# Kernel optimization log

Hardware: AMD Instinct MI355X
Metric: run time of the kernel (lower is better)

The kernel has to match this reference:

```python
import jax, jax.numpy as jnp
import numpy as np

X_DIM, Y_DIM, HIDDEN, N = 768, 768, 300, 768


def setup_inputs() -> dict:
    key = jax.random.key(0)
    ks = jax.random.split(key, 7)
    lim1 = 1.0 / np.sqrt(X_DIM + Y_DIM)
    lim2 = 1.0 / np.sqrt(HIDDEN)
    return {
        "x_samples": jax.random.normal(ks[0], (N, X_DIM), dtype=jnp.float32),
        "y_samples": jax.random.normal(ks[1], (N, Y_DIM), dtype=jnp.float32),
        "perm": jax.random.permutation(ks[2], N).astype(jnp.int32),
        # Linear 1: (x_dim+y_dim) -> hidden, torch default uniform init
        "W1": jax.random.uniform(ks[3], (HIDDEN, X_DIM + Y_DIM), jnp.float32, -lim1, lim1),
        "b1": jax.random.uniform(ks[4], (HIDDEN,), jnp.float32, -lim1, lim1),
        # Linear 2: hidden -> 1
        "W2": jax.random.uniform(ks[5], (1, HIDDEN), jnp.float32, -lim2, lim2),
        "b2": jax.random.uniform(ks[6], (1,), jnp.float32, -lim2, lim2),
    }


def reference(x_samples, y_samples, perm, W1, b1, W2, b2):
    n = x_samples.shape[0]
    x_dim = x_samples.shape[1]
    # First linear is separable across the concat: split W1 into x- and y-parts.
    hx = x_samples @ W1[:, :x_dim].T            # [N, H]
    hy = y_samples @ W1[:, x_dim:].T            # [N, H]
    w2 = W2[0]                                   # [H]
    # T0: matched pairs (x_i, y_i)
    t0 = jax.nn.softplus(jax.nn.relu(hx + hy + b1) @ w2 + b2[0])   # [N]
    # T1[i, j] = F(x_j, y_perm[i]) -- pairwise tile, [N, N, H] intermediate
    hyp = hy[perm]                               # [N, H]
    hpair = jax.nn.relu(hyp[:, None, :] + hx[None, :, :] + b1)     # [N, N, H]
    t1 = jax.nn.softplus(hpair @ w2 + b2[0])     # [N, N]
    lower_bound = t0.mean() - (jax.nn.logsumexp(t1, axis=1).mean() - jnp.log(n).astype(t1.dtype))
    return lower_bound
```

## Files before the change

kernel.cpp:

```cpp
#include <hip/hip_runtime.h>
#include <math.h>

#define NN   768
#define HH   300
#define KD   768

#define P_OFF    0
#define PKS_STR  245760
#define PG_STR   1966080
#define CF_OFF   3932160
#define AF_OFF   4177920
#define RS_OFF   4423680
#define T0_OFF   4435968

__global__ __launch_bounds__(256) void k1_gemm(
    const float* __restrict__ x, const float* __restrict__ y,
    const int* __restrict__ perm, const float* __restrict__ W1,
    float* __restrict__ wsf)
{
    const int tid = threadIdx.x;
    const int tx = tid & 15;
    const int ty = tid >> 4;
    const int i0 = blockIdx.x * 128;
    const int h0 = blockIdx.y * 64;
    const int g  = blockIdx.z & 1;
    const int ks = blockIdx.z >> 1;
    const int kbeg = ks * 96;

    const float* src = g ? y : x;
    const int koff = g ? KD : 0;

    __shared__ float Xt[32][132];
    __shared__ float Wt[32][68];

    float4 acc[4][2];
    #pragma unroll
    for (int r = 0; r < 4; ++r) { acc[r][0] = make_float4(0,0,0,0);
                                  acc[r][1] = make_float4(0,0,0,0); }

    const int kq = (tid & 7) << 2;
    const float* xp[4];
    int xr[4];
    #pragma unroll
    for (int it = 0; it < 4; ++it) {
        int row = ((tid + it*256) >> 3);
        int gr = i0 + row;
        if (g) gr = perm[gr];
        xp[it] = src + (size_t)gr * KD + kbeg + kq;
        xr[it] = row;
    }
    const float* wp[2];
    int wr[2]; bool wv[2];
    #pragma unroll
    for (int it = 0; it < 2; ++it) {
        int hrow = ((tid + it*256) >> 3);
        int hg = h0 + hrow;
        wv[it] = hg < HH;
        wp[it] = W1 + (size_t)(wv[it] ? hg : 0) * (2*KD) + koff + kbeg + kq;
        wr[it] = hrow;
    }

    for (int kb = 0; kb < 96; kb += 32) {
        float4 xv[4], wvv[2];
        #pragma unroll
        for (int it = 0; it < 4; ++it) xv[it] = *(const float4*)(xp[it] + kb);
        #pragma unroll
        for (int it = 0; it < 2; ++it) {
            wvv[it] = *(const float4*)(wp[it] + kb);
            if (!wv[it]) wvv[it] = make_float4(0,0,0,0);
        }
        if (kb) __syncthreads();
        #pragma unroll
        for (int it = 0; it < 4; ++it) {
            Xt[kq+0][xr[it]] = xv[it].x; Xt[kq+1][xr[it]] = xv[it].y;
            Xt[kq+2][xr[it]] = xv[it].z; Xt[kq+3][xr[it]] = xv[it].w;
        }
        #pragma unroll
        for (int it = 0; it < 2; ++it) {
            Wt[kq+0][wr[it]] = wvv[it].x; Wt[kq+1][wr[it]] = wvv[it].y;
            Wt[kq+2][wr[it]] = wvv[it].z; Wt[kq+3][wr[it]] = wvv[it].w;
        }
        __syncthreads();

        #pragma unroll 8
        for (int k = 0; k < 32; ++k) {
            float4 a  = *(const float4*)&Wt[k][4*ty];
            float4 b0 = *(const float4*)&Xt[k][4*tx];
            float4 b1v = *(const float4*)&Xt[k][64 + 4*tx];
            float ar[4] = {a.x, a.y, a.z, a.w};
            #pragma unroll
            for (int r = 0; r < 4; ++r) {
                acc[r][0].x = fmaf(ar[r], b0.x,  acc[r][0].x);
                acc[r][0].y = fmaf(ar[r], b0.y,  acc[r][0].y);
                acc[r][0].z = fmaf(ar[r], b0.z,  acc[r][0].z);
                acc[r][0].w = fmaf(ar[r], b0.w,  acc[r][0].w);
                acc[r][1].x = fmaf(ar[r], b1v.x, acc[r][1].x);
                acc[r][1].y = fmaf(ar[r], b1v.y, acc[r][1].y);
                acc[r][1].z = fmaf(ar[r], b1v.z, acc[r][1].z);
                acc[r][1].w = fmaf(ar[r], b1v.w, acc[r][1].w);
            }
        }
    }

    float* dst = wsf + P_OFF + (size_t)(g*8 + ks) * PKS_STR;
    #pragma unroll
    for (int r = 0; r < 4; ++r) {
        float* rp = dst + (size_t)(h0 + 4*ty + r) * NN + i0;
        *(float4*)(rp + 4*tx)      = acc[r][0];
        *(float4*)(rp + 64 + 4*tx) = acc[r][1];
    }
}

__global__ __launch_bounds__(256) void k1b_combine(
    const float* __restrict__ b1, float* __restrict__ wsf)
{
    int idx = blockIdx.x * 256 + threadIdx.x;
    int g = idx >= 61440;
    int rem = idx - g * 61440;
    int h = rem / 192;
    int i4 = (rem % 192) * 4;

    float4 o = make_float4(0.f,0.f,0.f,0.f);
    if (h < HH) {
        const float* p = wsf + P_OFF + (size_t)g * PG_STR + (size_t)h * NN + i4;
        #pragma unroll
        for (int ks = 0; ks < 8; ++ks) {
            float4 v = *(const float4*)(p + (size_t)ks * PKS_STR);
            o.x += v.x; o.y += v.y; o.z += v.z; o.w += v.w;
        }
        if (g) {
            float bv = b1[h];
            o.x += bv; o.y += bv; o.z += bv; o.w += bv;
        }
    }
    float* dst = wsf + (g ? AF_OFF : CF_OFF) + (size_t)h * NN + i4;
    *(float4*)dst = o;
}

__global__ __launch_bounds__(256) void k2_pair(
    const float* __restrict__ wsf, const float* __restrict__ w2,
    const int* __restrict__ perm, const float* __restrict__ b2,
    float* __restrict__ rsO, float* __restrict__ t0c)
{
    const int tid = threadIdx.x;
    const int tx = tid & 15;
    const int ty = tid >> 4;
    const int j0 = blockIdx.x * 48;
    const int i0 = blockIdx.y * 48;

    const float* AF = wsf + AF_OFF;
    const float* CF = wsf + CF_OFF;

    __shared__ float As[50][48];
    __shared__ float Cs[50][48];
    __shared__ float w2s[50];

    int ho[3], qo[3]; bool val[3];
    #pragma unroll
    for (int s = 0; s < 3; ++s) {
        int e = tid + s * 256;
        val[s] = e < 600;
        ho[s] = e / 12;
        qo[s] = (e % 12) * 4;
    }

    float acc[3][3];
    #pragma unroll
    for (int r = 0; r < 3; ++r)
        #pragma unroll
        for (int c = 0; c < 3; ++c) acc[r][c] = 0.f;

    float4 pa[3] = {}, pc[3] = {};
    #pragma unroll
    for (int s = 0; s < 3; ++s) if (val[s]) {
        pa[s] = *(const float4*)(AF + (size_t)ho[s] * NN + i0 + qo[s]);
        pc[s] = *(const float4*)(CF + (size_t)ho[s] * NN + j0 + qo[s]);
    }
    float pw = (tid < 50) ? w2[tid] : 0.f;

    for (int cc = 0; cc < 6; ++cc) {
        if (cc) __syncthreads();
        #pragma unroll
        for (int s = 0; s < 3; ++s) if (val[s]) {
            *(float4*)&As[ho[s]][qo[s]] = pa[s];
            *(float4*)&Cs[ho[s]][qo[s]] = pc[s];
        }
        if (tid < 50) w2s[tid] = pw;
        __syncthreads();

        if (cc < 5) {
            const float* a = AF + (size_t)(cc + 1) * 50 * NN;
            const float* c = CF + (size_t)(cc + 1) * 50 * NN;
            #pragma unroll
            for (int s = 0; s < 3; ++s) if (val[s]) {
                pa[s] = *(const float4*)(a + (size_t)ho[s] * NN + i0 + qo[s]);
                pc[s] = *(const float4*)(c + (size_t)ho[s] * NN + j0 + qo[s]);
            }
            if (tid < 50) pw = w2[(cc + 1) * 50 + tid];
        }

        #pragma unroll 5
        for (int h = 0; h < 50; ++h) {
            float wh = w2s[h];
            float ar[3] = {As[h][ty], As[h][ty + 16], As[h][ty + 32]};
            float cr[3] = {Cs[h][tx], Cs[h][tx + 16], Cs[h][tx + 32]};
            #pragma unroll
            for (int r = 0; r < 3; ++r)
                #pragma unroll
                for (int c = 0; c < 3; ++c)
                    acc[r][c] = fmaf(fmaxf(ar[r] + cr[c], 0.f), wh, acc[r][c]);
        }
    }

    const float b2v = b2[0];
    #pragma unroll
    for (int r = 0; r < 3; ++r) {
        int i = i0 + ty + 16 * r;
        int pj = perm[i];
        float rsum = 0.f;
        #pragma unroll
        for (int c = 0; c < 3; ++c) {
            int j = j0 + tx + 16 * c;
            float u = acc[r][c] + b2v;
            rsum += expf(u);
            if (j == pj)
                t0c[i] = (u > 0.f) ? u + log1pf(expf(-u)) : log1pf(expf(u));
        }
        #pragma unroll
        for (int off = 8; off; off >>= 1)
            rsum += __shfl_xor(rsum, off, 16);
        if (tx == 0) rsO[(size_t)blockIdx.x * NN + i] = rsum;
    }
}

__global__ __launch_bounds__(256) void k3_final(
    const float* __restrict__ wsf, float* __restrict__ out)
{
    const int tid = threadIdx.x;
    const float* rs = wsf + RS_OFF;
    const float* t0 = wsf + T0_OFF;

    double st0 = 0.0, slse = 0.0;
    for (int i = tid; i < NN; i += 256) {
        float s = 0.f;
        #pragma unroll
        for (int jb = 0; jb < 16; ++jb) s += rs[(size_t)jb * NN + i];
        st0  += (double)t0[i];
        slse += log((double)NN + (double)s);
    }
    __shared__ double sa[256], sb[256];
    sa[tid] = st0; sb[tid] = slse;
    __syncthreads();
    for (int s = 128; s > 0; s >>= 1) {
        if (tid < s) { sa[tid] += sa[tid+s]; sb[tid] += sb[tid+s]; }
        __syncthreads();
    }
    if (tid == 0) {
        double lb = sa[0]/(double)NN - (sb[0]/(double)NN - log((double)NN));
        out[0] = (float)lb;
    }
}

extern "C" void kernel_launch(void* const* d_in, const int* in_sizes, int n_in,
                              void* d_out, int out_size, void* d_ws, size_t ws_size,
                              hipStream_t stream) {
    const float* x    = (const float*)d_in[0];
    const float* y    = (const float*)d_in[1];
    const int*   perm = (const int*)  d_in[2];
    const float* W1   = (const float*)d_in[3];
    const float* b1   = (const float*)d_in[4];
    const float* W2   = (const float*)d_in[5];
    const float* b2   = (const float*)d_in[6];
    float* wsf = (float*)d_ws;
    float* out = (float*)d_out;

    k1_gemm    <<<dim3(6,5,16), 256, 0, stream>>>(x, y, perm, W1, wsf);
    k1b_combine<<<480,          256, 0, stream>>>(b1, wsf);
    k2_pair    <<<dim3(16,16),  256, 0, stream>>>(wsf, W2, perm, b2,
                                                  wsf + RS_OFF, wsf + T0_OFF);
    k3_final   <<<1,            256, 0, stream>>>(wsf, out);
}
```

Measured before the change: 129.1 us.

## Store hidden activations row-major with padded hidden dim for vectorized pair kernel

Changes the intermediate hx/hy buffers from hidden-major [H][N] to sample-major [N][320] with hidden padded to 320. The GEMM epilogue writes transposed float4s, the combine kernel reduces along the new layout, and the pair kernel loads whole hidden chunks of 152 per sample into shared memory and reads float4 along hidden. The aim is fewer shared-memory load instructions and fewer sync phases in the pair kernel (2 chunks instead of 6). The trade-off is larger shared memory per block (~60KB), which may lower occupancy, and possible bank conflicts with the 156-float row stride.

```diff
diff --git a/kernel.cpp b/kernel.cpp
--- a/kernel.cpp
+++ b/kernel.cpp
@@ -3,6 +3,7 @@
 
 #define NN   768
 #define HH   300
+#define HP   320
 #define KD   768
 
 #define P_OFF    0
@@ -33,10 +34,11 @@
     __shared__ float Xt[32][132];
     __shared__ float Wt[32][68];
 
-    float4 acc[4][2];
-    #pragma unroll
-    for (int r = 0; r < 4; ++r) { acc[r][0] = make_float4(0,0,0,0);
-                                  acc[r][1] = make_float4(0,0,0,0); }
+    float acc[4][8];
+    #pragma unroll
+    for (int r = 0; r < 4; ++r)
+        #pragma unroll
+        for (int cc = 0; cc < 8; ++cc) acc[r][cc] = 0.f;
 
     const int kq = (tid & 7) << 2;
     const float* xp[4];
@@ -88,26 +90,21 @@
             float4 b0 = *(const float4*)&Xt[k][4*tx];
             float4 b1v = *(const float4*)&Xt[k][64 + 4*tx];
             float ar[4] = {a.x, a.y, a.z, a.w};
+            float br[8] = {b0.x, b0.y, b0.z, b0.w, b1v.x, b1v.y, b1v.z, b1v.w};
             #pragma unroll
-            for (int r = 0; r < 4; ++r) {
-                acc[r][0].x = fmaf(ar[r], b0.x,  acc[r][0].x);
-                acc[r][0].y = fmaf(ar[r], b0.y,  acc[r][0].y);
-                acc[r][0].z = fmaf(ar[r], b0.z,  acc[r][0].z);
-                acc[r][0].w = fmaf(ar[r], b0.w,  acc[r][0].w);
-                acc[r][1].x = fmaf(ar[r], b1v.x, acc[r][1].x);
-                acc[r][1].y = fmaf(ar[r], b1v.y, acc[r][1].y);
-                acc[r][1].z = fmaf(ar[r], b1v.z, acc[r][1].z);
-                acc[r][1].w = fmaf(ar[r], b1v.w, acc[r][1].w);
-            }
+            for (int r = 0; r < 4; ++r)
+                #pragma unroll
+                for (int cc = 0; cc < 8; ++cc)
+                    acc[r][cc] = fmaf(ar[r], br[cc], acc[r][cc]);
         }
     }
 
     float* dst = wsf + P_OFF + (size_t)(g*8 + ks) * PKS_STR;
     #pragma unroll
-    for (int r = 0; r < 4; ++r) {
-        float* rp = dst + (size_t)(h0 + 4*ty + r) * NN + i0;
-        *(float4*)(rp + 4*tx)      = acc[r][0];
-        *(float4*)(rp + 64 + 4*tx) = acc[r][1];
+    for (int cc = 0; cc < 8; ++cc) {
+        int i = i0 + ((cc >> 2) ? 64 : 0) + 4*tx + (cc & 3);
+        float4 v = make_float4(acc[0][cc], acc[1][cc], acc[2][cc], acc[3][cc]);
+        *(float4*)(dst + (size_t)i * HP + h0 + 4*ty) = v;
     }
 }
 
@@ -117,23 +114,21 @@
     int idx = blockIdx.x * 256 + threadIdx.x;
     int g = idx >= 61440;
     int rem = idx - g * 61440;
-    int h = rem / 192;
-    int i4 = (rem % 192) * 4;
+    int i = rem / 80;
+    int h4 = (rem % 80) * 4;
 
     float4 o = make_float4(0.f,0.f,0.f,0.f);
-    if (h < HH) {
-        const float* p = wsf + P_OFF + (size_t)g * PG_STR + (size_t)h * NN + i4;
-        #pragma unroll
-        for (int ks = 0; ks < 8; ++ks) {
-            float4 v = *(const float4*)(p + (size_t)ks * PKS_STR);
-            o.x += v.x; o.y += v.y; o.z += v.z; o.w += v.w;
-        }
-        if (g) {
-            float bv = b1[h];
-            o.x += bv; o.y += bv; o.z += bv; o.w += bv;
-        }
-    }
-    float* dst = wsf + (g ? AF_OFF : CF_OFF) + (size_t)h * NN + i4;
+    const float* p = wsf + P_OFF + (size_t)g * PG_STR + (size_t)i * HP + h4;
+    #pragma unroll
+    for (int ks = 0; ks < 8; ++ks) {
+        float4 v = *(const float4*)(p + (size_t)ks * PKS_STR);
+        o.x += v.x; o.y += v.y; o.z += v.z; o.w += v.w;
+    }
+    if (g && h4 < HH) {
+        float4 bv = *(const float4*)(b1 + h4);
+        o.x += bv.x; o.y += bv.y; o.z += bv.z; o.w += bv.w;
+    }
+    float* dst = wsf + (g ? AF_OFF : CF_OFF) + (size_t)i * HP + h4;
     *(float4*)dst = o;
 }
 
@@ -151,17 +146,14 @@
     const float* AF = wsf + AF_OFF;
     const float* CF = wsf + CF_OFF;
 
-    __shared__ float As[50][48];
-    __shared__ float Cs[50][48];
-    __shared__ float w2s[50];
-
-    int ho[3], qo[3]; bool val[3];
-    #pragma unroll
-    for (int s = 0; s < 3; ++s) {
-        int e = tid + s * 256;
-        val[s] = e < 600;
-        ho[s] = e / 12;
-        qo[s] = (e % 12) * 4;
+    __shared__ __align__(16) float As[48][156];
+    __shared__ __align__(16) float Cs[48][156];
+    __shared__ __align__(16) float w2s[304];
+
+    if (tid < 76) {
+        float4 wv = make_float4(0.f,0.f,0.f,0.f);
+        if (tid < 75) wv = *(const float4*)(w2 + 4*tid);
+        *(float4*)&w2s[4*tid] = wv;
     }
 
     float acc[3][3];
@@ -170,45 +162,51 @@
         #pragma unroll
         for (int c = 0; c < 3; ++c) acc[r][c] = 0.f;
 
-    float4 pa[3] = {}, pc[3] = {};
-    #pragma unroll
-    for (int s = 0; s < 3; ++s) if (val[s]) {
-        pa[s] = *(const float4*)(AF + (size_t)ho[s] * NN + i0 + qo[s]);
-        pc[s] = *(const float4*)(CF + (size_t)ho[s] * NN + j0 + qo[s]);
-    }
-    float pw = (tid < 50) ? w2[tid] : 0.f;
-
-    for (int cc = 0; cc < 6; ++cc) {
-        if (cc) __syncthreads();
-        #pragma unroll
-        for (int s = 0; s < 3; ++s) if (val[s]) {
-            *(float4*)&As[ho[s]][qo[s]] = pa[s];
-            *(float4*)&Cs[ho[s]][qo[s]] = pc[s];
-        }
-        if (tid < 50) w2s[tid] = pw;
+    #pragma unroll
+    for (int ch = 0; ch < 2; ++ch) {
+        const int hbeg = ch * 152;
+        const int nq = ch ? 37 : 38;
+        if (ch) __syncthreads();
+        for (int e = tid; e < 48 * nq; e += 256) {
+            int i = e / nq, q = e % nq;
+            *(float4*)&As[i][4*q] =
+                *(const float4*)(AF + (size_t)(i0 + i) * HP + hbeg + 4*q);
+            *(float4*)&Cs[i][4*q] =
+                *(const float4*)(CF + (size_t)(j0 + i) * HP + hbeg + 4*q);
+        }
         __syncthreads();
 
-        if (cc < 5) {
-            const float* a = AF + (size_t)(cc + 1) * 50 * NN;
-            const float* c = CF + (size_t)(cc + 1) * 50 * NN;
+        #pragma unroll 2
+        for (int k = 0; k < nq; ++k) {
+            float4 wq = *(const float4*)&w2s[hbeg + 4*k];
+            float4 a0 = *(const float4*)&As[ty     ][4*k];
+            float4 a1 = *(const float4*)&As[ty + 16][4*k];
+            float4 a2 = *(const float4*)&As[ty + 32][4*k];
+            float4 c0 = *(const float4*)&Cs[tx     ][4*k];
+            float4 c1 = *(const float4*)&Cs[tx + 16][4*k];
+            float4 c2 = *(const float4*)&Cs[tx + 32][4*k];
+            const float* wp = (const float*)&wq;
+            const float* ap0 = (const float*)&a0;
+            const float* ap1 = (const float*)&a1;
+            const float* ap2 = (const float*)&a2;
+            const float* cp0 = (const float*)&c0;
+            const float* cp1 = (const float*)&c1;
+            const float* cp2 = (const float*)&c2;
             #pragma unroll
-            for (int s = 0; s < 3; ++s) if (val[s]) {
-                pa[s] = *(const float4*)(a + (size_t)ho[s] * NN + i0 + qo[s]);
-                pc[s] = *(const float4*)(c + (size_t)ho[s] * NN + j0 + qo[s]);
+            for (int hh = 0; hh < 4; ++hh) {
+                float wh = wp[hh];
+                float av0 = ap0[hh], av1 = ap1[hh], av2 = ap2[hh];
+                float cv0 = cp0[hh], cv1 = cp1[hh], cv2 = cp2[hh];
+                acc[0][0] = fmaf(fmaxf(av0 + cv0, 0.f), wh, acc[0][0]);
+                acc[0][1] = fmaf(fmaxf(av0 + cv1, 0.f), wh, acc[0][1]);
+                acc[0][2] = fmaf(fmaxf(av0 + cv2, 0.f), wh, acc[0][2]);
+                acc[1][0] = fmaf(fmaxf(av1 + cv0, 0.f), wh, acc[1][0]);
+                acc[1][1] = fmaf(fmaxf(av1 + cv1, 0.f), wh, acc[1][1]);
+                acc[1][2] = fmaf(fmaxf(av1 + cv2, 0.f), wh, acc[1][2]);
+                acc[2][0] = fmaf(fmaxf(av2 + cv0, 0.f), wh, acc[2][0]);
+                acc[2][1] = fmaf(fmaxf(av2 + cv1, 0.f), wh, acc[2][1]);
+                acc[2][2] = fmaf(fmaxf(av2 + cv2, 0.f), wh, acc[2][2]);
             }
-            if (tid < 50) pw = w2[(cc + 1) * 50 + tid];
-        }
-
-        #pragma unroll 5
-        for (int h = 0; h < 50; ++h) {
-            float wh = w2s[h];
-            float ar[3] = {As[h][ty], As[h][ty + 16], As[h][ty + 32]};
-            float cr[3] = {Cs[h][tx], Cs[h][tx + 16], Cs[h][tx + 32]};
-            #pragma unroll
-            for (int r = 0; r < 3; ++r)
-                #pragma unroll
-                for (int c = 0; c < 3; ++c)
-                    acc[r][c] = fmaf(fmaxf(ar[r] + cr[c], 0.f), wh, acc[r][c]);
         }
     }
 
```

Measured after the change: 117.4 us. 9.1% less time.
